# Performance work log

Measured on AMD Instinct MI355X. Metric: run time of the kernel, lower is better.

Reference implementation:

```python
import jax, jax.numpy as jnp
import numpy as np

BINS = 10  # constructor default


def setup_inputs() -> dict:
    key = jax.random.key(0)
    k1, k2 = jax.random.split(key)
    bs, cla = 262144, 128
    # probabilities strictly inside (0,1) so log terms are finite
    u = jax.random.uniform(k1, (bs, cla), dtype=jnp.float32)
    inputs = 0.01 + 0.98 * u
    # binary 0/1 targets as floats
    targets = jnp.round(jax.random.uniform(k2, (bs, cla), dtype=jnp.float32))
    return {"inputs": inputs, "targets": targets}


def reference(inputs, targets):
    bins = BINS
    tot = jnp.asarray(inputs.size, jnp.float32)  # bs * cla

    # gradient-norm proxy g = |p.detach() - t|, in [0, 1]
    g = jnp.abs(jax.lax.stop_gradient(inputs) - targets)

    # edges are i/bins with the last edge nudged to 1+1e-6, so
    # floor(g*bins) clipped to bins-1 reproduces the per-bin masks exactly
    idx = jnp.clip(jnp.floor(g * bins).astype(jnp.int32), 0, bins - 1)

    # histogram counts per bin (fused scatter-add instead of the Python loop)
    counts = jnp.zeros((bins,), jnp.float32).at[idx.ravel()].add(1.0)

    n = jnp.sum(counts > 0).astype(jnp.float32)  # number of non-empty bins
    w_per_bin = jnp.where(counts > 0, tot / jnp.maximum(counts, 1.0), 0.0)
    weights = w_per_bin[idx] / jnp.maximum(n, 1.0)
    weights = jax.lax.stop_gradient(weights)  # weights built from detached g

    # elementwise binary cross entropy on probabilities
    bce = -(targets * jnp.log(inputs) + (1.0 - targets) * jnp.log1p(-inputs))
    loss = jnp.sum(weights * bce) / tot
    return loss
```

## Files before the change

### kernel.cpp

```cpp
#include <hip/hip_runtime.h>

#define BINS 10

__device__ __forceinline__ void elem(float p, float t,
                                     float* __restrict__ sb,
                                     unsigned int* __restrict__ cw)
{
    float g  = fabsf(p - t);
    float l2 = __log2f(1.0f - g);
    int   bi = (int)(g * 10.0f);
#pragma unroll
    for (int b = 0; b < BINS; ++b) {
        bool hit = (bi == b);
        unsigned long long m = __ballot(hit);
        sb[b] += hit ? l2 : 0.0f;
        cw[b] += (unsigned int)__popcll(m);
    }
}

__device__ __forceinline__ void proc4v(const float4 p, const float4 t,
                                       float* __restrict__ sb,
                                       unsigned int* __restrict__ cw)
{
    elem(p.x, t.x, sb, cw); elem(p.y, t.y, sb, cw);
    elem(p.z, t.z, sb, cw); elem(p.w, t.w, sb, cw);
}

__global__ __launch_bounds__(256, 4) void ghm_partial(
    const float4* __restrict__ p4,
    const float4* __restrict__ t4,
    float* __restrict__ gsum,
    unsigned int* __restrict__ gcnt,
    int n4)
{
    float        sb[BINS];
    unsigned int cw[BINS];
#pragma unroll
    for (int b = 0; b < BINS; ++b) { sb[b] = 0.0f; cw[b] = 0u; }

    const int tid    = threadIdx.x;
    const int start  = blockIdx.x * blockDim.x + tid;
    const int stride = gridDim.x * blockDim.x;
    const int ngrp   = n4 / (4 * stride);

    int i = start;
    for (int grp = 0; grp < ngrp; ++grp, i += 4 * stride) {
        float4 P0 = p4[i];
        float4 T0 = t4[i];
        float4 P1 = p4[i + stride];
        float4 T1 = t4[i + stride];
        float4 P2 = p4[i + 2 * stride];
        float4 T2 = t4[i + 2 * stride];
        float4 P3 = p4[i + 3 * stride];
        float4 T3 = t4[i + 3 * stride];
        __builtin_amdgcn_sched_barrier(0);
        proc4v(P0, T0, sb, cw);
        proc4v(P1, T1, sb, cw);
        proc4v(P2, T2, sb, cw);
        proc4v(P3, T3, sb, cw);
    }
    for (int j = start + ngrp * 4 * stride; j < n4; j += stride) {
        float4 p = p4[j], t = t4[j];
        proc4v(p, t, sb, cw);
    }

    __shared__ float        redS[BINS];
    __shared__ unsigned int redC[BINS];
    if (tid < BINS) { redS[tid] = 0.0f; redC[tid] = 0u; }
    __syncthreads();

    const int lane = tid & 63;
#pragma unroll
    for (int b = 0; b < BINS; ++b) {
        float s = sb[b];
#pragma unroll
        for (int off = 32; off > 0; off >>= 1) s += __shfl_down(s, off);
        if (lane == 0) {
            atomicAdd(&redS[b], s);
            atomicAdd(&redC[b], cw[b]);
        }
    }
    __syncthreads();
    if (tid < BINS) {
        atomicAdd(&gsum[tid], redS[tid]);
        atomicAdd(&gcnt[tid], redC[tid]);
    }
}

__global__ void ghm_finalize(const float* __restrict__ gsum,
                             const unsigned int* __restrict__ gcnt,
                             float* __restrict__ out)
{
    if (threadIdx.x == 0 && blockIdx.x == 0) {
        int n = 0;
#pragma unroll
        for (int b = 0; b < BINS; ++b) n += (gcnt[b] > 0u) ? 1 : 0;
        float nn = (float)(n > 0 ? n : 1);
        float acc = 0.0f;
#pragma unroll
        for (int b = 0; b < BINS; ++b) {
            if (gcnt[b] > 0u)
                acc += gsum[b] / ((float)gcnt[b] * nn);
        }
        out[0] = -0.6931471805599453f * acc;
    }
}

extern "C" void kernel_launch(void* const* d_in, const int* in_sizes, int n_in,
                              void* d_out, int out_size, void* d_ws, size_t ws_size,
                              hipStream_t stream)
{
    const float* p = (const float*)d_in[0];
    const float* t = (const float*)d_in[1];
    const int n  = in_sizes[0];
    const int n4 = n >> 2;

    float*        gsum = (float*)d_ws;
    unsigned int* gcnt = (unsigned int*)((char*)d_ws + BINS * sizeof(float));

    hipMemsetAsync(d_ws, 0, BINS * (sizeof(float) + sizeof(unsigned int)), stream);

    const int threads = 256;
    const int blocks  = 2048;
    ghm_partial<<<blocks, threads, 0, stream>>>(
        (const float4*)p, (const float4*)t, gsum, gcnt, n4);

    ghm_finalize<<<1, 64, 0, stream>>>(gsum, gcnt, (float*)d_out);
}
```

Baseline: 292.9 us.

## Stream inputs through LDS with async global_load_lds and a 4-deep per-wave pipeline

Replaces direct register float4 loads with asynchronous global-to-LDS loads (global_load_lds), organised as a 4-stage ring buffer per wave so several chunks are in flight while earlier ones are being processed. Explicit vmcnt waits gate each chunk before it is consumed. The aim is to keep more memory requests outstanding and hide load latency in this bandwidth-bound reduction. In exchange it adds LDS use (32 KB per block), which may limit occupancy, drops the min-blocks launch bound, and depends on vmcnt counting being correct.

```diff
diff --git a/kernel.cpp b/kernel.cpp
--- a/kernel.cpp
+++ b/kernel.cpp
@@ -1,6 +1,20 @@
 #include <hip/hip_runtime.h>
 
-#define BINS 10
+#define BINS  10
+#define DEPTH 4
+#define WPB   4
+#define CHUNK 64
+
+typedef float f4 __attribute__((ext_vector_type(4)));
+
+typedef __attribute__((address_space(1))) void gvoid;
+typedef __attribute__((address_space(3))) void lvoid;
+
+__device__ __forceinline__ void async16(const f4* g, f4* l) {
+    __builtin_amdgcn_global_load_lds((gvoid*)g, (lvoid*)l, 16, 0, 0);
+}
+
+#define WAITVM(N) asm volatile("s_waitcnt vmcnt(" #N ")" ::: "memory")
 
 __device__ __forceinline__ void elem(float p, float t,
                                      float* __restrict__ sb,
@@ -18,7 +32,7 @@
     }
 }
 
-__device__ __forceinline__ void proc4v(const float4 p, const float4 t,
+__device__ __forceinline__ void proc4v(const f4 p, const f4 t,
                                        float* __restrict__ sb,
                                        unsigned int* __restrict__ cw)
 {
@@ -26,50 +40,71 @@
     elem(p.z, t.z, sb, cw); elem(p.w, t.w, sb, cw);
 }
 
-__global__ __launch_bounds__(256, 4) void ghm_partial(
-    const float4* __restrict__ p4,
-    const float4* __restrict__ t4,
+__global__ __launch_bounds__(256) void ghm_partial(
+    const f4* __restrict__ p4,
+    const f4* __restrict__ t4,
     float* __restrict__ gsum,
     unsigned int* __restrict__ gcnt,
     int n4)
 {
+    __shared__ f4 lsp[WPB][DEPTH][CHUNK];
+    __shared__ f4 lst[WPB][DEPTH][CHUNK];
+
     float        sb[BINS];
     unsigned int cw[BINS];
 #pragma unroll
     for (int b = 0; b < BINS; ++b) { sb[b] = 0.0f; cw[b] = 0u; }
 
-    const int tid    = threadIdx.x;
-    const int start  = blockIdx.x * blockDim.x + tid;
-    const int stride = gridDim.x * blockDim.x;
-    const int ngrp   = n4 / (4 * stride);
+    const int tid  = threadIdx.x;
+    const int w    = tid >> 6;
+    const int lane = tid & 63;
+    const int wave_global  = blockIdx.x * WPB + w;
+    const int total_waves  = gridDim.x * WPB;
+    const long cs  = (long)total_waves * CHUNK;
+    const int  NC  = (int)(n4 / cs);
 
-    int i = start;
-    for (int grp = 0; grp < ngrp; ++grp, i += 4 * stride) {
-        float4 P0 = p4[i];
-        float4 T0 = t4[i];
-        float4 P1 = p4[i + stride];
-        float4 T1 = t4[i + stride];
-        float4 P2 = p4[i + 2 * stride];
-        float4 T2 = t4[i + 2 * stride];
-        float4 P3 = p4[i + 3 * stride];
-        float4 T3 = t4[i + 3 * stride];
-        __builtin_amdgcn_sched_barrier(0);
-        proc4v(P0, T0, sb, cw);
-        proc4v(P1, T1, sb, cw);
-        proc4v(P2, T2, sb, cw);
-        proc4v(P3, T3, sb, cw);
+    const f4* pg = p4 + (long)wave_global * CHUNK + lane;
+    const f4* tg = t4 + (long)wave_global * CHUNK + lane;
+
+#define ISSUE(k) do { int _s = (k) & (DEPTH - 1);                        \
+        async16(pg + (long)(k) * cs, &lsp[w][_s][0]);                    \
+        async16(tg + (long)(k) * cs, &lst[w][_s][0]); } while (0)
+
+#define CONSUME(k) do { int _s = (k) & (DEPTH - 1);                      \
+        f4 _p = lsp[w][_s][lane];                                        \
+        f4 _t = lst[w][_s][lane];                                        \
+        proc4v(_p, _t, sb, cw); } while (0)
+
+    if (NC >= DEPTH) {
+        ISSUE(0); ISSUE(1); ISSUE(2); ISSUE(3);
+        for (int k = 0; k < NC - DEPTH; ++k) {
+            WAITVM(6);
+            CONSUME(k);
+            ISSUE(k + DEPTH);
+        }
+        WAITVM(6); CONSUME(NC - 4);
+        WAITVM(4); CONSUME(NC - 3);
+        WAITVM(2); CONSUME(NC - 2);
+        WAITVM(0); CONSUME(NC - 1);
+    } else {
+        for (int k = 0; k < NC; ++k) {
+            f4 p = pg[(long)k * cs];
+            f4 t = tg[(long)k * cs];
+            proc4v(p, t, sb, cw);
+        }
     }
-    for (int j = start + ngrp * 4 * stride; j < n4; j += stride) {
-        float4 p = p4[j], t = t4[j];
-        proc4v(p, t, sb, cw);
-    }
+    for (long j = NC * cs + blockIdx.x * blockDim.x + tid; j < n4;
+         j += (long)gridDim.x * blockDim.x)
+        proc4v(p4[j], t4[j], sb, cw);
+
+#undef ISSUE
+#undef CONSUME
 
     __shared__ float        redS[BINS];
     __shared__ unsigned int redC[BINS];
     if (tid < BINS) { redS[tid] = 0.0f; redC[tid] = 0u; }
     __syncthreads();
 
-    const int lane = tid & 63;
 #pragma unroll
     for (int b = 0; b < BINS; ++b) {
         float s = sb[b];
@@ -123,7 +158,7 @@
     const int threads = 256;
     const int blocks  = 2048;
     ghm_partial<<<blocks, threads, 0, stream>>>(
-        (const float4*)p, (const float4*)t, gsum, gcnt, n4);
+        (const f4*)p, (const f4*)t, gsum, gcnt, n4);
 
     ghm_finalize<<<1, 64, 0, stream>>>(gsum, gcnt, (float*)d_out);
 }
```

Measured after the change: 300.3 us. +2.5%, slower.
